# Kernel optimization log

Measured on AMD Instinct MI355X. Metric: run time of the kernel, lower is better.

The kernel has to match this reference:

```python
import jax, jax.numpy as jnp
import numpy as np

N = 50000      # nodes
E = 800000     # random edges (self-loops added in reference, as PyG GATConv does)
G = 1024       # graphs in the batch
F_IN = 35      # num_features_xd
H1, C1 = 10, 35   # gcn1: heads=10, out=35 -> concat 350
H2, C2 = 1, 128   # gcn2: heads=1, out=128
NEG_SLOPE = 0.2   # PyG GATConv default leaky_relu slope


def setup_inputs() -> dict:
    key = jax.random.key(0)
    ks = jax.random.split(key, 16)
    g = lambda k, sh, fan: jax.random.normal(k, sh, jnp.float32) / jnp.sqrt(jnp.float32(fan))
    return {
        "x": jax.random.normal(ks[0], (N, F_IN), jnp.float32),
        "edge_index": jax.random.randint(ks[1], (2, E), 0, N),
        "batch": jnp.sort(jax.random.randint(ks[2], (N,), 0, G)),
        # gcn1 params
        "W1": g(ks[3], (F_IN, H1 * C1), F_IN),
        "att_src1": g(ks[4], (H1, C1), C1),
        "att_dst1": g(ks[5], (H1, C1), C1),
        "b1": jnp.zeros((H1 * C1,), jnp.float32),
        # gcn2 params
        "W2": g(ks[6], (H1 * C1, H2 * C2), H1 * C1),
        "att_src2": g(ks[7], (H2, C2), C2),
        "att_dst2": g(ks[8], (H2, C2), C2),
        "b2": jnp.zeros((H2 * C2,), jnp.float32),
        # dense head
        "Wg": g(ks[9], (C2, C2), C2),
        "bg": jnp.zeros((C2,), jnp.float32),
        "Wo": g(ks[10], (C2, 1), C2),
        "bo": jnp.zeros((1,), jnp.float32),
    }


def _gat_conv(x, src, dst, W, att_src, att_dst, b, heads, ch):
    """PyG GATConv (eval mode): edge attention + segment softmax + scatter sum."""
    h = (x @ W).reshape(-1, heads, ch)                      # [N,H,C]
    a_s = jnp.einsum('nhc,hc->nh', h, att_src)              # [N,H]
    a_d = jnp.einsum('nhc,hc->nh', h, att_dst)
    e = jax.nn.leaky_relu(a_s[src] + a_d[dst], NEG_SLOPE)   # [Etot,H]
    m = jax.ops.segment_max(e, dst, num_segments=N)         # segment softmax over dst
    ex = jnp.exp(e - m[dst])
    den = jax.ops.segment_sum(ex, dst, num_segments=N)
    alpha = ex / den[dst]                                   # [Etot,H]
    out = jax.ops.segment_sum(alpha[:, :, None] * h[src], dst, num_segments=N)
    return out.reshape(-1, heads * ch) + b                  # concat heads + bias


def reference(x, edge_index, batch, W1, att_src1, att_dst1, b1,
              W2, att_src2, att_dst2, b2, Wg, bg, Wo, bo):
    # add self-loops (PyG GATConv default add_self_loops=True)
    loop = jnp.arange(N, dtype=edge_index.dtype)
    src = jnp.concatenate([edge_index[0], loop])
    dst = jnp.concatenate([edge_index[1], loop])

    h = jax.nn.elu(_gat_conv(x, src, dst, W1, att_src1, att_dst1, b1, H1, C1))
    h = jax.nn.relu(_gat_conv(h, src, dst, W2, att_src2, att_dst2, b2, H2, C2))

    # global max pool over graphs
    pooled = jax.ops.segment_max(h, batch, num_segments=G)
    pooled = jnp.where(jnp.isneginf(pooled), 0.0, pooled)   # guard empty graphs

    z = jax.nn.relu(pooled @ Wg + bg)
    return z @ Wo + bo                                      # [G, 1]
```

## Files before the change

### kernel.cpp

```cpp
#include <hip/hip_runtime.h>
#include <hip/hip_bf16.h>
#include <cmath>

#define N_NODES 50000
#define N_EDGES 800000
#define N_GRAPHS 1024
#define F_IN 35
#define H1 10
#define C1 35
#define HC1 350
#define C2 128
#define NB256 196

typedef unsigned int uint32;
typedef __attribute__((ext_vector_type(8))) short short8;
typedef __attribute__((ext_vector_type(4))) float f32x4;

static __device__ __forceinline__ float bflo(uint32 u) { return __uint_as_float(u << 16); }
static __device__ __forceinline__ float bfhi(uint32 u) { return __uint_as_float(u & 0xffff0000u); }
static __device__ __forceinline__ unsigned short bfbits(float f) {
    return __builtin_bit_cast(unsigned short, __float2bfloat16(f));
}
static __device__ __forceinline__ uint32 packbf(float a, float b) {
    return ((uint32)bfbits(b) << 16) | (uint32)bfbits(a);
}
static __device__ __forceinline__ float lrelu(float e) { return (e > 0.f) ? e : 0.2f * e; }

__global__ void k_count(const int* __restrict__ dst, int* __restrict__ deg) {
    int e = blockIdx.x * blockDim.x + threadIdx.x;
    if (e < N_EDGES) atomicAdd(&deg[dst[e]], 1);
}

__global__ __launch_bounds__(256) void k_bsum(const int* __restrict__ deg, int* __restrict__ bsum) {
    const int i = blockIdx.x * 256 + threadIdx.x;
    int v = (i < N_NODES) ? deg[i] : 0;
#pragma unroll
    for (int off = 32; off; off >>= 1) v += __shfl_xor(v, off);
    __shared__ int ws[4];
    if ((threadIdx.x & 63) == 0) ws[threadIdx.x >> 6] = v;
    __syncthreads();
    if (threadIdx.x == 0) bsum[blockIdx.x] = ws[0] + ws[1] + ws[2] + ws[3];
}

__global__ __launch_bounds__(256) void k_bscan(const int* __restrict__ bsum, int* __restrict__ bpre) {
    __shared__ int buf[256];
    const int t = threadIdx.x;
    int v = (t < NB256) ? bsum[t] : 0;
    buf[t] = v;
    __syncthreads();
    for (int off = 1; off < 256; off <<= 1) {
        int u = (t >= off) ? buf[t - off] : 0;
        __syncthreads();
        buf[t] += u;
        __syncthreads();
    }
    if (t < NB256) bpre[t] = buf[t] - v;
}

__global__ __launch_bounds__(256) void k_boffs(const int* __restrict__ deg,
                                               const int* __restrict__ bpre,
                                               int* __restrict__ offs, int* __restrict__ cursor) {
    const int b = blockIdx.x, t = threadIdx.x;
    const int i = b * 256 + t;
    const int lane = t & 63, wid = t >> 6;
    int v = (i < N_NODES) ? deg[i] : 0;
    int s = v;
#pragma unroll
    for (int off = 1; off < 64; off <<= 1) {
        int u = __shfl_up(s, off);
        if (lane >= off) s += u;
    }
    __shared__ int wsum[4];
    if (lane == 63) wsum[wid] = s;
    __syncthreads();
    int wbase = 0;
    for (int w = 0; w < wid; ++w) wbase += wsum[w];
    int excl = bpre[b] + wbase + s - v;
    if (i < N_NODES) { offs[i] = excl; cursor[i] = excl; }
    if (i == 0) offs[N_NODES] = N_EDGES;
}

__global__ void k_fill(const int* __restrict__ src, const int* __restrict__ dst,
                       int* __restrict__ cursor, int* __restrict__ csr) {
    int e = blockIdx.x * blockDim.x + threadIdx.x;
    if (e < N_EDGES) {
        int p = atomicAdd(&cursor[dst[e]], 1);
        csr[p] = src[e];
    }
}

#define XB ((N_NODES * 5 + 255) / 256)
__global__ __launch_bounds__(256) void k_prep(const float* __restrict__ x,
                                              const float* __restrict__ W1,
                                              const float* __restrict__ attS1,
                                              const float* __restrict__ attD1,
                                              const float* __restrict__ b1,
                                              const float* __restrict__ W2,
                                              uint32* __restrict__ xbf,
                                              float* __restrict__ fold,
                                              uint32* __restrict__ W1g,
                                              uint32* __restrict__ W2f) {
    const int b = blockIdx.x, t = threadIdx.x;
    if (b < XB) {
        int idx = b * 256 + t;
        if (idx >= N_NODES * 5) return;
        int n = idx / 5, s = idx - n * 5;
        uint32 o[4];
#pragma unroll
        for (int p = 0; p < 4; ++p) {
            int ch0 = s * 8 + 2 * p, ch1 = ch0 + 1;
            float a = (ch0 < F_IN) ? x[(size_t)n * F_IN + ch0] : (ch0 == 35 ? 1.f : 0.f);
            float bb = (ch1 < F_IN) ? x[(size_t)n * F_IN + ch1] : (ch1 == 35 ? 1.f : 0.f);
            o[p] = packbf(a, bb);
        }
        uint32* d = xbf + (size_t)idx * 4;
        d[0] = o[0]; d[1] = o[1]; d[2] = o[2]; d[3] = o[3];
    } else if (b < XB + 3) {
        int idx = (b - XB) * 256 + t;
        if (idx >= 700) return;
        int k = idx / 20, o = idx - k * 20;
        int h = (o < 10) ? o : o - 10;
        const float* att = (o < 10) ? attS1 : attD1;
        float s = 0.f;
        for (int c = 0; c < C1; ++c)
            s = fmaf(W1[k * HC1 + h * C1 + c], att[h * C1 + c], s);
        fold[k * 20 + o] = s;
    } else if (b < XB + 3 + 15) {
        int idx = (b - XB - 3) * 256 + t;
        if (idx >= 10 * 2 * 3 * 64) return;
        int lane = idx & 63;
        int rest = idx >> 6;
        int tt = rest % 3;
        int rest2 = rest / 3;
        int kk = rest2 & 1;
        int h = rest2 >> 1;
        int c = tt * 16 + (lane & 15);
        int k0 = kk * 32 + (lane >> 4) * 8;
        uint32 o[4];
#pragma unroll
        for (int jj = 0; jj < 4; ++jj) {
            float v[2];
#pragma unroll
            for (int half = 0; half < 2; ++half) {
                int k = k0 + 2 * jj + half;
                float val = 0.f;
                if (c < C1) {
                    if (k < F_IN) val = W1[k * HC1 + h * C1 + c];
                    else if (k == 35) val = b1[h * C1 + c];
                }
                v[half] = val;
            }
            o[jj] = packbf(v[0], v[1]);
        }
        uint32* d = W1g + (size_t)idx * 4;
        d[0] = o[0]; d[1] = o[1]; d[2] = o[2]; d[3] = o[3];
    } else {
        int idx = (b - XB - 3 - 15) * 256 + t;
        if (idx >= 11 * 8 * 64) return;
        int lane = idx & 63;
        int tt = (idx >> 6) & 7;
        int kk = idx >> 9;
        int c = tt * 16 + (lane & 15);
        int k0 = kk * 32 + (lane >> 4) * 8;
        uint32 o[4];
#pragma unroll
        for (int jj = 0; jj < 4; ++jj) {
            int ka = k0 + 2 * jj, kb = ka + 1;
            float va = (ka < HC1) ? W2[ka * C2 + c] : 0.f;
            float vb = (kb < HC1) ? W2[kb * C2 + c] : 0.f;
            o[jj] = packbf(va, vb);
        }
        uint32* d = W2f + (size_t)idx * 4;
        d[0] = o[0]; d[1] = o[1]; d[2] = o[2]; d[3] = o[3];
    }
}

__global__ __launch_bounds__(256) void k_att1(const float* __restrict__ x,
                                              const float* __restrict__ fold,
                                              float* __restrict__ a_s1,
                                              float* __restrict__ a_d1) {
    int idx = blockIdx.x * 256 + threadIdx.x;
    if (idx >= N_NODES * 20) return;
    int n = idx / 20, o = idx - n * 20;
    const float* xr = x + (size_t)n * F_IN;
    float acc = 0.f;
#pragma unroll
    for (int k = 0; k < F_IN; ++k) acc = fmaf(xr[k], fold[k * 20 + o], acc);
    if (o < 10) a_s1[n * 10 + o] = acc;
    else        a_d1[n * 10 + (o - 10)] = acc;
}

__global__ __launch_bounds__(256, 8) void k_aggx(const uint4* __restrict__ xbf4,
                                                 const float* __restrict__ a_s,
                                                 const float* __restrict__ a_d,
                                                 const int* __restrict__ offs,
                                                 const int* __restrict__ csr,
                                                 uint4* __restrict__ aggx4) {
    __shared__ float al[4][10][68];
    __shared__ float addl[4][10];
    __shared__ int totmax[4];
    const int tid = threadIdx.x, lane = tid & 63, wid = tid >> 6;
    const int d = blockIdx.x * 4 + wid;
    const int o0 = offs[d];
    const int deg = offs[d + 1] - o0;
    const int total = deg + 1;
    const int g = lane >> 4, u = lane & 15;
    const int hg = (u >= 10) ? 2 : ((u >= 5) ? 1 : 0);
    const int sl = u - hg * 5;
    const bool act = (u < 15);
    const int h0 = hg * 4;

    if (lane < 10) addl[wid][lane] = a_d[(size_t)d * 10 + lane];
    if (lane < 4) {
#pragma unroll
        for (int h = 0; h < 10; ++h) al[wid][h][64 + lane] = 0.f;
    }
    if (lane == 0) totmax[wid] = total;
    __syncthreads();
    const int tmx = max(max(totmax[0], totmax[1]), max(totmax[2], totmax[3]));
    const int rounds = (tmx + 63) >> 6;

    float acc[4][8];
#pragma unroll
    for (int a = 0; a < 4; ++a)
#pragma unroll
        for (int q = 0; q < 8; ++q) acc[a][q] = 0.f;

    for (int rb = 0; rb < rounds; ++rb) {
        const int base = rb << 6;
        const int i = base + lane;
        int s_mine = d;
        if (i < total) {
            if (i < deg) s_mine = __builtin_nontemporal_load(csr + o0 + i);
            const float2* ap = (const float2*)(a_s + (size_t)s_mine * 10);
            float2 p0 = ap[0], p1 = ap[1], p2 = ap[2], p3 = ap[3], p4 = ap[4];
            al[wid][0][lane] = __expf(lrelu(p0.x + addl[wid][0]));
            al[wid][1][lane] = __expf(lrelu(p0.y + addl[wid][1]));
            al[wid][2][lane] = __expf(lrelu(p1.x + addl[wid][2]));
            al[wid][3][lane] = __expf(lrelu(p1.y + addl[wid][3]));
            al[wid][4][lane] = __expf(lrelu(p2.x + addl[wid][4]));
            al[wid][5][lane] = __expf(lrelu(p2.y + addl[wid][5]));
            al[wid][6][lane] = __expf(lrelu(p3.x + addl[wid][6]));
            al[wid][7][lane] = __expf(lrelu(p3.y + addl[wid][7]));
            al[wid][8][lane] = __expf(lrelu(p4.x + addl[wid][8]));
            al[wid][9][lane] = __expf(lrelu(p4.y + addl[wid][9]));
        } else {
#pragma unroll
            for (int h = 0; h < 10; ++h) al[wid][h][lane] = 0.f;
        }
        __syncthreads();
        const int cnt = min(64, total - base);
        if (cnt > 0) {
            uint4 v0 = {0, 0, 0, 0}, v1 = {0, 0, 0, 0};
            {
                int s0 = __shfl(s_mine, g);
                if (act) v0 = xbf4[(size_t)s0 * 5 + sl];
            }
            if (4 < cnt) {
                int s1 = __shfl(s_mine, 4 + g);
                if (act) v1 = xbf4[(size_t)s1 * 5 + sl];
            }
            for (int jb = 0; jb < cnt; jb += 4) {
                uint4 w = v0;
                v0 = v1;
                const int jj = jb + g;
                if (jb + 8 < cnt) {
                    int sn = __shfl(s_mine, jb + 8 + g);
                    if (act) v1 = xbf4[(size_t)sn * 5 + sl];
                }
                float f0 = bflo(w.x), f1 = bfhi(w.x), f2 = bflo(w.y), f3 = bfhi(w.y);
                float f4 = bflo(w.z), f5 = bfhi(w.z), f6 = bflo(w.w), f7 = bfhi(w.w);
#pragma unroll
                for (int a = 0; a < 4; ++a) {
                    const int hidx = min(h0 + a, 9);
                    const float aj = al[wid][hidx][jj];
                    acc[a][0] = fmaf(aj, f0, acc[a][0]);
                    acc[a][1] = fmaf(aj, f1, acc[a][1]);
                    acc[a][2] = fmaf(aj, f2, acc[a][2]);
                    acc[a][3] = fmaf(aj, f3, acc[a][3]);
                    acc[a][4] = fmaf(aj, f4, acc[a][4]);
                    acc[a][5] = fmaf(aj, f5, acc[a][5]);
                    acc[a][6] = fmaf(aj, f6, acc[a][6]);
                    acc[a][7] = fmaf(aj, f7, acc[a][7]);
                }
            }
        }
        __syncthreads();
    }
#pragma unroll
    for (int a = 0; a < 4; ++a)
#pragma unroll
        for (int q = 0; q < 8; ++q) {
            acc[a][q] += __shfl_xor(acc[a][q], 16);
            acc[a][q] += __shfl_xor(acc[a][q], 32);
        }
    const int nh = (hg == 2) ? 2 : 4;
#pragma unroll
    for (int a = 0; a < 4; ++a) {
        float den = __shfl(acc[a][3], hg * 5 + 4);
        float rdn = 1.f / den;
        if (g == 0 && act && a < nh) {
            uint4 ov;
            ov.x = packbf(acc[a][0] * rdn, acc[a][1] * rdn);
            ov.y = packbf(acc[a][2] * rdn, acc[a][3] * rdn);
            ov.z = packbf(acc[a][4] * rdn, acc[a][5] * rdn);
            ov.w = packbf(acc[a][6] * rdn, acc[a][7] * rdn);
            aggx4[((size_t)d * 10 + h0 + a) * 5 + sl] = ov;
        }
    }
}

__global__ __launch_bounds__(256, 8) void k_gemm1b(const short* __restrict__ aggx,
                                                   const short8* __restrict__ W1g,
                                                   unsigned short* __restrict__ x2p) {
    const int lane = threadIdx.x & 63;
    const int wid = threadIdx.x >> 6;
    const int mtile = blockIdx.x * 4 + wid;
    if (mtile >= N_NODES / 16) return;
    const int c_lo = lane & 15, grp = lane >> 4;
    const int m0 = mtile * 16;
    const size_t abase = (size_t)(m0 + c_lo) * 400 + grp * 8;

#pragma unroll
    for (int h = 0; h < 10; ++h) {
        const short* ap = aggx + abase + h * 40;
        short8 a0 = *reinterpret_cast<const short8*>(ap);
        short8 a1 = *reinterpret_cast<const short8*>(ap + 32);
        f32x4 acc[3];
#pragma unroll
        for (int tt = 0; tt < 3; ++tt) acc[tt] = (f32x4){0.f, 0.f, 0.f, 0.f};
#pragma unroll
        for (int tt = 0; tt < 3; ++tt)
            acc[tt] = __builtin_amdgcn_mfma_f32_16x16x32_bf16(a0, W1g[((h * 2 + 0) * 3 + tt) * 64 + lane], acc[tt], 0, 0, 0);
#pragma unroll
        for (int tt = 0; tt < 3; ++tt)
            acc[tt] = __builtin_amdgcn_mfma_f32_16x16x32_bf16(a1, W1g[((h * 2 + 1) * 3 + tt) * 64 + lane], acc[tt], 0, 0, 0);
#pragma unroll
        for (int tt = 0; tt < 3; ++tt) {
            int c = tt * 16 + c_lo;
            if (c < C1) {
#pragma unroll
                for (int r = 0; r < 4; ++r) {
                    int node = m0 + grp * 4 + r;
                    float v = acc[tt][r];
                    v = (v > 0.f) ? v : expm1f(v);
                    x2p[(size_t)node * 352 + h * C1 + c] = bfbits(v);
                }
            }
        }
    }
    if (lane < 16) ((uint32*)x2p)[(size_t)(m0 + lane) * 176 + 175] = 0u;
}

__global__ __launch_bounds__(256) void k_gemm2(const short* __restrict__ x2p,
                                               const short8* __restrict__ W2f,
                                               const float* __restrict__ attS,
                                               const float* __restrict__ attD,
                                               unsigned short* __restrict__ h2b,
                                               float* __restrict__ a_s2, float* __restrict__ a_d2) {
    const int lane = threadIdx.x & 63;
    const int wid = threadIdx.x >> 6;
    const int mtile = blockIdx.x * 4 + wid;
    if (mtile >= N_NODES / 16) return;
    const int c_lo = lane & 15, grp = lane >> 4;
    const int m0 = mtile * 16;
    const short* aptr = x2p + (size_t)(m0 + c_lo) * 352 + grp * 8;

    f32x4 acc[8];
#pragma unroll
    for (int t = 0; t < 8; ++t) acc[t] = (f32x4){0.f, 0.f, 0.f, 0.f};
#pragma unroll
    for (int kk = 0; kk < 11; ++kk) {
        short8 a = *reinterpret_cast<const short8*>(aptr + kk * 32);
#pragma unroll
        for (int t = 0; t < 8; ++t) {
            short8 b = W2f[(kk * 8 + t) * 64 + lane];
            acc[t] = __builtin_amdgcn_mfma_f32_16x16x32_bf16(a, b, acc[t], 0, 0, 0);
        }
    }
    float attSv[8], attDv[8];
#pragma unroll
    for (int t = 0; t < 8; ++t) {
        attSv[t] = attS[t * 16 + c_lo];
        attDv[t] = attD[t * 16 + c_lo];
    }
    float ps[4] = {0, 0, 0, 0}, pd[4] = {0, 0, 0, 0};
#pragma unroll
    for (int t = 0; t < 8; ++t)
#pragma unroll
        for (int r = 0; r < 4; ++r) {
            ps[r] = fmaf(acc[t][r], attSv[t], ps[r]);
            pd[r] = fmaf(acc[t][r], attDv[t], pd[r]);
        }
#pragma unroll
    for (int r = 0; r < 4; ++r) {
        int node = m0 + grp * 4 + r;
#pragma unroll
        for (int t = 0; t < 8; ++t) h2b[(size_t)node * C2 + t * 16 + c_lo] = bfbits(acc[t][r]);
    }
#pragma unroll
    for (int r = 0; r < 4; ++r) {
        float s = ps[r], dd = pd[r];
#pragma unroll
        for (int off = 1; off < 16; off <<= 1) {
            s += __shfl_xor(s, off);
            dd += __shfl_xor(dd, off);
        }
        if (c_lo == 0) {
            int node = m0 + grp * 4 + r;
            a_s2[node] = s;
            a_d2[node] = dd;
        }
    }
}

__global__ __launch_bounds__(256, 8) void k_agg2(const uint4* __restrict__ feat4,
                                                 const float* __restrict__ a_s,
                                                 const float* __restrict__ a_d,
                                                 const int* __restrict__ offs,
                                                 const int* __restrict__ csr,
                                                 const float* __restrict__ b2,
                                                 float* __restrict__ out2) {
    const int lane = threadIdx.x & 63;
    const int wid = threadIdx.x >> 6;
    const int d = blockIdx.x * 4 + wid;
    const int o0 = offs[d];
    const int deg = offs[d + 1] - o0;
    const int total = deg + 1;
    const float add = a_d[d];
    const int g = lane >> 4, cl = lane & 15;

    float acc[8];
#pragma unroll
    for (int q = 0; q < 8; ++q) acc[q] = 0.f;
    float den = 0.f;

    for (int base = 0; base < total; base += 64) {
        const int i = base + lane;
        int s_mine = d;
        float e_mine = 0.f;
        if (i < total) {
            if (i < deg) s_mine = __builtin_nontemporal_load(csr + o0 + i);
            e_mine = __expf(lrelu(a_s[s_mine] + add));
            den += e_mine;
        }
        const int cnt = min(64, total - base);
        float aj0 = __shfl(e_mine, g);
        uint4 v0 = feat4[(size_t)__shfl(s_mine, g) * 16 + cl];
        float aj1 = 0.f;
        uint4 v1 = {0, 0, 0, 0};
        if (4 < cnt) {
            aj1 = __shfl(e_mine, 4 + g);
            v1 = feat4[(size_t)__shfl(s_mine, 4 + g) * 16 + cl];
        }
        for (int jb = 0; jb < cnt; jb += 4) {
            uint4 v = v0;
            float a = aj0;
            v0 = v1; aj0 = aj1;
            if (jb + 8 < cnt) {
                int ni = jb + 8 + g;
                aj1 = __shfl(e_mine, ni);
                v1 = feat4[(size_t)__shfl(s_mine, ni) * 16 + cl];
            }
            acc[0] = fmaf(a, bflo(v.x), acc[0]);
            acc[1] = fmaf(a, bfhi(v.x), acc[1]);
            acc[2] = fmaf(a, bflo(v.y), acc[2]);
            acc[3] = fmaf(a, bfhi(v.y), acc[3]);
            acc[4] = fmaf(a, bflo(v.z), acc[4]);
            acc[5] = fmaf(a, bfhi(v.z), acc[5]);
            acc[6] = fmaf(a, bflo(v.w), acc[6]);
            acc[7] = fmaf(a, bfhi(v.w), acc[7]);
        }
    }
#pragma unroll
    for (int q = 0; q < 8; ++q) {
        acc[q] += __shfl_xor(acc[q], 16);
        acc[q] += __shfl_xor(acc[q], 32);
    }
#pragma unroll
    for (int off = 32; off > 0; off >>= 1) den += __shfl_xor(den, off);

    if (lane < 16) {
        const float rden = 1.f / den;
        const float4* bp = (const float4*)(b2 + 8 * cl);
        float4 b0 = bp[0], b1 = bp[1];
        float4 o0v, o1v;
        o0v.x = fmaxf(acc[0] * rden + b0.x, 0.f);
        o0v.y = fmaxf(acc[1] * rden + b0.y, 0.f);
        o0v.z = fmaxf(acc[2] * rden + b0.z, 0.f);
        o0v.w = fmaxf(acc[3] * rden + b0.w, 0.f);
        o1v.x = fmaxf(acc[4] * rden + b1.x, 0.f);
        o1v.y = fmaxf(acc[5] * rden + b1.y, 0.f);
        o1v.z = fmaxf(acc[6] * rden + b1.z, 0.f);
        o1v.w = fmaxf(acc[7] * rden + b1.w, 0.f);
        float4* op = (float4*)(out2 + (size_t)d * C2 + 8 * cl);
        op[0] = o0v;
        op[1] = o1v;
    }
}

__global__ __launch_bounds__(128) void k_pool(const float* __restrict__ out2,
                                              const int* __restrict__ batch,
                                              float* __restrict__ pooled) {
    const int c = threadIdx.x;
    const int n0 = blockIdx.x * 50;
    const int n1 = min(n0 + 50, N_NODES);
    int curB = batch[n0];
    float curM = 0.f;
    float v = out2[(size_t)n0 * C2 + c];
    for (int n = n0; n < n1; ++n) {
        float cur = v;
        int b = batch[n];
        if (n + 1 < n1) v = out2[(size_t)(n + 1) * C2 + c];
        if (b != curB) {
            atomicMax((int*)&pooled[curB * C2 + c], __float_as_int(curM));
            curB = b;
            curM = cur;
        } else {
            curM = fmaxf(curM, cur);
        }
    }
    atomicMax((int*)&pooled[curB * C2 + c], __float_as_int(curM));
}

__global__ __launch_bounds__(128) void k_head(const float* __restrict__ pooled,
                                              const float* __restrict__ Wg,
                                              const float* __restrict__ bg,
                                              const float* __restrict__ Wo,
                                              const float* __restrict__ bo,
                                              float* __restrict__ out) {
    __shared__ float p[C2];
    __shared__ float wsum[2];
    const int g = blockIdx.x;
    const int tid = threadIdx.x;
    p[tid] = pooled[g * C2 + tid];
    __syncthreads();
    float acc = bg[tid];
#pragma unroll 8
    for (int k = 0; k < C2; ++k) acc = fmaf(p[k], Wg[k * C2 + tid], acc);
    float z = fmaxf(acc, 0.f);
    float prod = z * Wo[tid];
#pragma unroll
    for (int off = 32; off; off >>= 1) prod += __shfl_down(prod, off);
    if ((tid & 63) == 0) wsum[tid >> 6] = prod;
    __syncthreads();
    if (tid == 0) out[g] = wsum[0] + wsum[1] + bo[0];
}

extern "C" void kernel_launch(void* const* d_in, const int* in_sizes, int n_in,
                              void* d_out, int out_size, void* d_ws, size_t ws_size,
                              hipStream_t stream) {
    const float* x        = (const float*)d_in[0];
    const int*   ei       = (const int*)d_in[1];
    const int*   batch    = (const int*)d_in[2];
    const float* W1       = (const float*)d_in[3];
    const float* att_src1 = (const float*)d_in[4];
    const float* att_dst1 = (const float*)d_in[5];
    const float* b1       = (const float*)d_in[6];
    const float* W2       = (const float*)d_in[7];
    const float* att_src2 = (const float*)d_in[8];
    const float* att_dst2 = (const float*)d_in[9];
    const float* b2       = (const float*)d_in[10];
    const float* Wg       = (const float*)d_in[11];
    const float* bg       = (const float*)d_in[12];
    const float* Wo       = (const float*)d_in[13];
    const float* bo       = (const float*)d_in[14];
    const int* src = ei;
    const int* dst = ei + N_EDGES;

    char* ws = (char*)d_ws;
    size_t off = 0;
    auto alloc = [&](size_t bytes) -> char* {
        char* p = ws + off;
        off = (off + bytes + 255) & ~(size_t)255;
        return p;
    };
    int*    deg    = (int*)alloc((size_t)N_NODES * 4);
    int*    offs   = (int*)alloc((size_t)(N_NODES + 1) * 4);
    int*    cursor = (int*)alloc((size_t)N_NODES * 4);
    int*    csr    = (int*)alloc((size_t)N_EDGES * 4);
    int*    bsum   = (int*)alloc((size_t)NB256 * 4);
    int*    bpre   = (int*)alloc((size_t)NB256 * 4);
    float*  a_s1   = (float*)alloc((size_t)N_NODES * H1 * 4);
    float*  a_d1   = (float*)alloc((size_t)N_NODES * H1 * 4);
    float*  a_s2   = (float*)alloc((size_t)N_NODES * 4);
    float*  a_d2   = (float*)alloc((size_t)N_NODES * 4);
    float*  pooled = (float*)alloc((size_t)N_GRAPHS * C2 * 4);
    float*  fold   = (float*)alloc((size_t)700 * 4);
    uint32* xbf    = (uint32*)alloc((size_t)N_NODES * 20 * 4);
    short*  aggx   = (short*)alloc((size_t)N_NODES * 400 * 2 + 256);
    uint32* x2p    = (uint32*)alloc((size_t)N_NODES * 176 * 4);
    unsigned short* h2b = (unsigned short*)alloc((size_t)N_NODES * C2 * 2);
    uint32* W1g    = (uint32*)alloc((size_t)10 * 2 * 3 * 64 * 16);
    uint32* W2f    = (uint32*)alloc((size_t)11 * 8 * 64 * 16);
    float*  out2   = (float*)aggx;

    hipMemsetAsync(deg, 0, (size_t)N_NODES * 4, stream);
    hipMemsetAsync(pooled, 0, (size_t)N_GRAPHS * C2 * 4, stream);

    k_count<<<(N_EDGES + 255) / 256, 256, 0, stream>>>(dst, deg);
    k_bsum<<<NB256, 256, 0, stream>>>(deg, bsum);
    k_bscan<<<1, 256, 0, stream>>>(bsum, bpre);
    k_boffs<<<NB256, 256, 0, stream>>>(deg, bpre, offs, cursor);
    k_fill<<<(N_EDGES + 255) / 256, 256, 0, stream>>>(src, dst, cursor, csr);

    k_prep<<<XB + 3 + 15 + 22, 256, 0, stream>>>(x, W1, att_src1, att_dst1, b1, W2,
                                                 xbf, fold, W1g, W2f);
    k_att1<<<(N_NODES * 20 + 255) / 256, 256, 0, stream>>>(x, fold, a_s1, a_d1);

    k_aggx<<<N_NODES / 4, 256, 0, stream>>>((const uint4*)xbf, a_s1, a_d1, offs, csr,
                                            (uint4*)aggx);

    k_gemm1b<<<(N_NODES / 16 + 3) / 4, 256, 0, stream>>>(aggx, (const short8*)W1g,
                                                         (unsigned short*)x2p);

    k_gemm2<<<(N_NODES / 16 + 3) / 4, 256, 0, stream>>>((const short*)x2p, (const short8*)W2f,
                                                        att_src2, att_dst2, h2b, a_s2, a_d2);

    k_agg2<<<N_NODES / 4, 256, 0, stream>>>((const uint4*)h2b, a_s2, a_d2, offs, csr, b2, out2);

    k_pool<<<(N_NODES + 49) / 50, 128, 0, stream>>>(out2, batch, pooled);

    k_head<<<N_GRAPHS, 128, 0, stream>>>(pooled, Wg, bg, Wo, bo, (float*)d_out);
}
```

Baseline: 367.5 us.

## Fuse layer-1 GEMM and ELU into the attention aggregation kernel

Removes the separate k_gemm1b pass. The aggregation kernel now stages each node's normalized 10x40 aggregated features in shared memory. It then computes the 350 projected outputs with scalar bf16×bf16 FMAs against a newly laid-out transposed W1, applies ELU and writes x2p directly. This eliminates the 40 MB aggx intermediate write/read and one kernel launch. In exchange, MFMA is replaced by per-lane scalar dot products, and every wave re-reads the full weight matrix through the cache.

```diff
diff --git a/kernel.cpp b/kernel.cpp
--- a/kernel.cpp
+++ b/kernel.cpp
@@ -18,6 +18,9 @@
 
 static __device__ __forceinline__ float bflo(uint32 u) { return __uint_as_float(u << 16); }
 static __device__ __forceinline__ float bfhi(uint32 u) { return __uint_as_float(u & 0xffff0000u); }
+static __device__ __forceinline__ float bfu(unsigned short u) {
+    return __uint_as_float((uint32)u << 16);
+}
 static __device__ __forceinline__ unsigned short bfbits(float f) {
     return __builtin_bit_cast(unsigned short, __float2bfloat16(f));
 }
@@ -98,7 +101,7 @@
                                               const float* __restrict__ W2,
                                               uint32* __restrict__ xbf,
                                               float* __restrict__ fold,
-                                              uint32* __restrict__ W1g,
+                                              uint32* __restrict__ W1t,
                                               uint32* __restrict__ W2f) {
     const int b = blockIdx.x, t = threadIdx.x;
     if (b < XB) {
@@ -125,37 +128,25 @@
         for (int c = 0; c < C1; ++c)
             s = fmaf(W1[k * HC1 + h * C1 + c], att[h * C1 + c], s);
         fold[k * 20 + o] = s;
-    } else if (b < XB + 3 + 15) {
+    } else if (b < XB + 3 + 7) {
         int idx = (b - XB - 3) * 256 + t;
-        if (idx >= 10 * 2 * 3 * 64) return;
-        int lane = idx & 63;
-        int rest = idx >> 6;
-        int tt = rest % 3;
-        int rest2 = rest / 3;
-        int kk = rest2 & 1;
-        int h = rest2 >> 1;
-        int c = tt * 16 + (lane & 15);
-        int k0 = kk * 32 + (lane >> 4) * 8;
-        uint32 o[4];
-#pragma unroll
-        for (int jj = 0; jj < 4; ++jj) {
-            float v[2];
-#pragma unroll
-            for (int half = 0; half < 2; ++half) {
-                int k = k0 + 2 * jj + half;
-                float val = 0.f;
-                if (c < C1) {
-                    if (k < F_IN) val = W1[k * HC1 + h * C1 + c];
-                    else if (k == 35) val = b1[h * C1 + c];
-                }
-                v[half] = val;
+        if (idx >= 352 * 5) return;
+        int o = idx / 5, s5 = idx - o * 5;
+        uint32 ov[4];
+#pragma unroll
+        for (int q = 0; q < 4; ++q) {
+            int k0 = s5 * 8 + 2 * q, k1 = k0 + 1;
+            float v0 = 0.f, v1 = 0.f;
+            if (o < HC1) {
+                v0 = (k0 < F_IN) ? W1[k0 * HC1 + o] : (k0 == 35 ? b1[o] : 0.f);
+                v1 = (k1 < F_IN) ? W1[k1 * HC1 + o] : (k1 == 35 ? b1[o] : 0.f);
             }
-            o[jj] = packbf(v[0], v[1]);
-        }
-        uint32* d = W1g + (size_t)idx * 4;
-        d[0] = o[0]; d[1] = o[1]; d[2] = o[2]; d[3] = o[3];
+            ov[q] = packbf(v0, v1);
+        }
+        uint32* d = W1t + (size_t)idx * 4;
+        d[0] = ov[0]; d[1] = ov[1]; d[2] = ov[2]; d[3] = ov[3];
     } else {
-        int idx = (b - XB - 3 - 15) * 256 + t;
+        int idx = (b - XB - 3 - 7) * 256 + t;
         if (idx >= 11 * 8 * 64) return;
         int lane = idx & 63;
         int tt = (idx >> 6) & 7;
@@ -190,15 +181,18 @@
     else        a_d1[n * 10 + (o - 10)] = acc;
 }
 
-__global__ __launch_bounds__(256, 8) void k_aggx(const uint4* __restrict__ xbf4,
+__global__ __launch_bounds__(256, 8) void k_aggp(const uint4* __restrict__ xbf4,
                                                  const float* __restrict__ a_s,
                                                  const float* __restrict__ a_d,
                                                  const int* __restrict__ offs,
                                                  const int* __restrict__ csr,
-                                                 uint4* __restrict__ aggx4) {
+                                                 const uint32* __restrict__ W1t,
+                                                 uint4* __restrict__ x2p4) {
     __shared__ float al[4][10][68];
     __shared__ float addl[4][10];
     __shared__ int totmax[4];
+    __shared__ uint32 stageu[4][200];
+    __shared__ unsigned short x2s[4][352];
     const int tid = threadIdx.x, lane = tid & 63, wid = tid >> 6;
     const int d = blockIdx.x * 4 + wid;
     const int o0 = offs[d];
@@ -300,56 +294,47 @@
         float den = __shfl(acc[a][3], hg * 5 + 4);
         float rdn = 1.f / den;
         if (g == 0 && act && a < nh) {
-            uint4 ov;
-            ov.x = packbf(acc[a][0] * rdn, acc[a][1] * rdn);
-            ov.y = packbf(acc[a][2] * rdn, acc[a][3] * rdn);
-            ov.z = packbf(acc[a][4] * rdn, acc[a][5] * rdn);
-            ov.w = packbf(acc[a][6] * rdn, acc[a][7] * rdn);
-            aggx4[((size_t)d * 10 + h0 + a) * 5 + sl] = ov;
-        }
-    }
-}
-
-__global__ __launch_bounds__(256, 8) void k_gemm1b(const short* __restrict__ aggx,
-                                                   const short8* __restrict__ W1g,
-                                                   unsigned short* __restrict__ x2p) {
-    const int lane = threadIdx.x & 63;
-    const int wid = threadIdx.x >> 6;
-    const int mtile = blockIdx.x * 4 + wid;
-    if (mtile >= N_NODES / 16) return;
-    const int c_lo = lane & 15, grp = lane >> 4;
-    const int m0 = mtile * 16;
-    const size_t abase = (size_t)(m0 + c_lo) * 400 + grp * 8;
-
-#pragma unroll
-    for (int h = 0; h < 10; ++h) {
-        const short* ap = aggx + abase + h * 40;
-        short8 a0 = *reinterpret_cast<const short8*>(ap);
-        short8 a1 = *reinterpret_cast<const short8*>(ap + 32);
-        f32x4 acc[3];
-#pragma unroll
-        for (int tt = 0; tt < 3; ++tt) acc[tt] = (f32x4){0.f, 0.f, 0.f, 0.f};
-#pragma unroll
-        for (int tt = 0; tt < 3; ++tt)
-            acc[tt] = __builtin_amdgcn_mfma_f32_16x16x32_bf16(a0, W1g[((h * 2 + 0) * 3 + tt) * 64 + lane], acc[tt], 0, 0, 0);
-#pragma unroll
-        for (int tt = 0; tt < 3; ++tt)
-            acc[tt] = __builtin_amdgcn_mfma_f32_16x16x32_bf16(a1, W1g[((h * 2 + 1) * 3 + tt) * 64 + lane], acc[tt], 0, 0, 0);
-#pragma unroll
-        for (int tt = 0; tt < 3; ++tt) {
-            int c = tt * 16 + c_lo;
-            if (c < C1) {
-#pragma unroll
-                for (int r = 0; r < 4; ++r) {
-                    int node = m0 + grp * 4 + r;
-                    float v = acc[tt][r];
-                    v = (v > 0.f) ? v : expm1f(v);
-                    x2p[(size_t)node * 352 + h * C1 + c] = bfbits(v);
-                }
+#pragma unroll
+            for (int q = 0; q < 4; ++q)
+                stageu[wid][(h0 + a) * 20 + sl * 4 + q] =
+                    packbf(acc[a][2 * q] * rdn, acc[a][2 * q + 1] * rdn);
+        }
+    }
+    __syncthreads();
+    const unsigned short* w1u = (const unsigned short*)W1t;
+#pragma unroll
+    for (int j = 0; j < 6; ++j) {
+        const int o = lane + 64 * j;
+        if (o < HC1) {
+            const int h = o / 35;
+            const uint32* sp = &stageu[wid][h * 20];
+            const short8* wp = (const short8*)(w1u + (size_t)o * 40);
+            float s = 0.f;
+#pragma unroll
+            for (int t8 = 0; t8 < 5; ++t8) {
+                short8 wv = wp[t8];
+                uint32 p0 = sp[t8 * 4 + 0], p1 = sp[t8 * 4 + 1];
+                uint32 p2 = sp[t8 * 4 + 2], p3 = sp[t8 * 4 + 3];
+                s = fmaf(bflo(p0), bfu((unsigned short)wv[0]), s);
+                s = fmaf(bfhi(p0), bfu((unsigned short)wv[1]), s);
+                s = fmaf(bflo(p1), bfu((unsigned short)wv[2]), s);
+                s = fmaf(bfhi(p1), bfu((unsigned short)wv[3]), s);
+                s = fmaf(bflo(p2), bfu((unsigned short)wv[4]), s);
+                s = fmaf(bfhi(p2), bfu((unsigned short)wv[5]), s);
+                s = fmaf(bflo(p3), bfu((unsigned short)wv[6]), s);
+                s = fmaf(bfhi(p3), bfu((unsigned short)wv[7]), s);
             }
-        }
-    }
-    if (lane < 16) ((uint32*)x2p)[(size_t)(m0 + lane) * 176 + 175] = 0u;
+            s = (s > 0.f) ? s : expm1f(s);
+            x2s[wid][o] = bfbits(s);
+        }
+    }
+    if (lane < 2) x2s[wid][350 + lane] = 0;
+    __syncthreads();
+    if (tid < 176) {
+        const int nodeI = tid / 44, slot = tid - nodeI * 44;
+        uint4 val = *(const uint4*)&x2s[nodeI][slot * 8];
+        x2p4[((size_t)(blockIdx.x * 4 + nodeI)) * 44 + slot] = val;
+    }
 }
 
 __global__ __launch_bounds__(256) void k_gemm2(const short* __restrict__ x2p,
@@ -588,12 +573,11 @@
     float*  pooled = (float*)alloc((size_t)N_GRAPHS * C2 * 4);
     float*  fold   = (float*)alloc((size_t)700 * 4);
     uint32* xbf    = (uint32*)alloc((size_t)N_NODES * 20 * 4);
-    short*  aggx   = (short*)alloc((size_t)N_NODES * 400 * 2 + 256);
     uint32* x2p    = (uint32*)alloc((size_t)N_NODES * 176 * 4);
     unsigned short* h2b = (unsigned short*)alloc((size_t)N_NODES * C2 * 2);
-    uint32* W1g    = (uint32*)alloc((size_t)10 * 2 * 3 * 64 * 16);
+    uint32* W1t    = (uint32*)alloc((size_t)352 * 5 * 16);
     uint32* W2f    = (uint32*)alloc((size_t)11 * 8 * 64 * 16);
-    float*  out2   = (float*)aggx;
+    float*  out2   = (float*)x2p;
 
     hipMemsetAsync(deg, 0, (size_t)N_NODES * 4, stream);
     hipMemsetAsync(pooled, 0, (size_t)N_GRAPHS * C2 * 4, stream);
@@ -604,15 +588,12 @@
     k_boffs<<<NB256, 256, 0, stream>>>(deg, bpre, offs, cursor);
     k_fill<<<(N_EDGES + 255) / 256, 256, 0, stream>>>(src, dst, cursor, csr);
 
-    k_prep<<<XB + 3 + 15 + 22, 256, 0, stream>>>(x, W1, att_src1, att_dst1, b1, W2,
-                                                 xbf, fold, W1g, W2f);
+    k_prep<<<XB + 3 + 7 + 22, 256, 0, stream>>>(x, W1, att_src1, att_dst1, b1, W2,
+                                                xbf, fold, W1t, W2f);
     k_att1<<<(N_NODES * 20 + 255) / 256, 256, 0, stream>>>(x, fold, a_s1, a_d1);
 
-    k_aggx<<<N_NODES / 4, 256, 0, stream>>>((const uint4*)xbf, a_s1, a_d1, offs, csr,
-                                            (uint4*)aggx);
-
-    k_gemm1b<<<(N_NODES / 16 + 3) / 4, 256, 0, stream>>>(aggx, (const short8*)W1g,
-                                                         (unsigned short*)x2p);
+    k_aggp<<<N_NODES / 4, 256, 0, stream>>>((const uint4*)xbf, a_s1, a_d1, offs, csr,
+                                            W1t, (uint4*)x2p);
 
     k_gemm2<<<(N_NODES / 16 + 3) / 4, 256, 0, stream>>>((const short*)x2p, (const short8*)W2f,
                                                         att_src2, att_dst2, h2b, a_s2, a_d2);
```

Measured after the change: 408.5 us. 1.11x slower.
